# Kernel optimization log

Measured on AMD Instinct MI355X. Metric: run time of the kernel, lower is better.

## Reference

```python
import jax, jax.numpy as jnp
import numpy as np

H, C = 2, 32            # n_heads, hidden_channels (GATv2Conv concat=False -> out dim C)
B, T_PER = 128, 1024    # graphs per batch, tasks per graph
N_TASKS = B * T_PER
N_DATA = 65536
E = 1048576             # edges per relation
N_DEV = 4
TASK_D, DATA_D, DEV_D, EDGE_D = 12, 5, 12, 3


def _leaky(x, s):
    return jnp.where(x >= 0, x, s * x)


def _layernorm(x, g, b):
    m = x.mean(-1, keepdims=True)
    v = x.var(-1, keepdims=True)
    return (x - m) / jnp.sqrt(v + 1e-5) * g + b


def _gatv2(x_src, x_dst, src, dst, Wl, bl, Wr, br, att, Wres, bias, n_dst,
           edge_attr=None, We=None):
    # PyG GATv2Conv: concat=False (mean over heads), residual=True, no self-loops.
    xl = (x_src @ Wl + bl).reshape(-1, H, C)   # [N_src, H, C]
    xr = (x_dst @ Wr + br).reshape(-1, H, C)   # [N_dst, H, C]
    m = xl[src] + xr[dst]                      # [E, H, C]
    if edge_attr is not None:
        m = m + (edge_attr @ We).reshape(-1, H, C)
    e = _leaky(m, 0.2)
    score = jnp.einsum('ehc,hc->eh', e, att)   # [E, H]
    smax = jax.ops.segment_max(score, dst, num_segments=n_dst)
    ex = jnp.exp(score - smax[dst])
    denom = jax.ops.segment_sum(ex, dst, num_segments=n_dst)
    alpha = ex / (denom[dst] + 1e-16)          # segment softmax per destination
    out = jax.ops.segment_sum(alpha[:, :, None] * xl[src], dst, num_segments=n_dst)
    return out.mean(axis=1) + x_dst @ Wres + bias


def setup_inputs() -> dict:
    key = jax.random.key(0)
    ks = iter(jax.random.split(key, 48))
    f = lambda shape: jax.random.normal(next(ks), shape, jnp.float32) * 0.1
    HC = H * C
    inp = {}
    inp['tasks_x'] = jax.random.normal(next(ks), (N_TASKS, TASK_D), jnp.float32)
    inp['data_x'] = jax.random.normal(next(ks), (N_DATA, DATA_D), jnp.float32)
    inp['devices_x'] = jax.random.normal(next(ks), (B * N_DEV, DEV_D), jnp.float32)
    src_dt = jax.random.randint(next(ks), (E,), 0, N_DATA)
    dst_dt = jax.random.randint(next(ks), (E,), 0, N_TASKS)
    inp['edge_index_dt'] = jnp.stack([src_dt, dst_dt])
    inp['edge_attr_dt'] = jax.random.normal(next(ks), (E, EDGE_D), jnp.float32)
    src_tt = jax.random.randint(next(ks), (E,), 0, N_TASKS)
    dst_tt = jax.random.randint(next(ks), (E,), 0, N_TASKS)
    inp['edge_index_tt'] = jnp.stack([src_tt, dst_tt])
    inp['batch'] = jnp.repeat(jnp.arange(B), T_PER)
    inp['ptr'] = jnp.arange(B) * T_PER
    inp['counts'] = jnp.full((B, 1), float(T_PER), jnp.float32)
    # conv1: (data -> tasks), with edge features
    inp['c1_Wl'] = f((DATA_D, HC)); inp['c1_bl'] = jnp.zeros(HC, jnp.float32)
    inp['c1_Wr'] = f((TASK_D, HC)); inp['c1_br'] = jnp.zeros(HC, jnp.float32)
    inp['c1_We'] = f((EDGE_D, HC)); inp['c1_att'] = f((H, C))
    inp['c1_Wres'] = f((TASK_D, C)); inp['c1_bias'] = jnp.zeros(C, jnp.float32)
    # conv2: (tasks -> tasks)
    inp['c2_Wl'] = f((TASK_D, HC)); inp['c2_bl'] = jnp.zeros(HC, jnp.float32)
    inp['c2_Wr'] = f((TASK_D, HC)); inp['c2_br'] = jnp.zeros(HC, jnp.float32)
    inp['c2_att'] = f((H, C))
    inp['c2_Wres'] = f((TASK_D, C)); inp['c2_bias'] = jnp.zeros(C, jnp.float32)
    inp['ln1_g'] = jnp.ones(C, jnp.float32); inp['ln1_b'] = jnp.zeros(C, jnp.float32)
    inp['ln2_g'] = jnp.ones(C, jnp.float32); inp['ln2_b'] = jnp.zeros(C, jnp.float32)
    gat_out = 2 * C + TASK_D                      # 76
    in_head = 2 * gat_out + N_DEV * DEV_D         # 200
    inp['h1_W'] = f((in_head, C)); inp['h1_b'] = jnp.zeros(C, jnp.float32)
    inp['hln_g'] = jnp.ones(C, jnp.float32); inp['hln_b'] = jnp.zeros(C, jnp.float32)
    inp['h2_W'] = f((C, N_DEV - 1)) * 0.01; inp['h2_b'] = jnp.zeros(N_DEV - 1, jnp.float32)
    return inp


def reference(tasks_x, data_x, devices_x, edge_attr_dt, counts,
              c1_Wl, c1_bl, c1_Wr, c1_br, c1_We, c1_att, c1_Wres, c1_bias,
              c2_Wl, c2_bl, c2_Wr, c2_br, c2_att, c2_Wres, c2_bias,
              ln1_g, ln1_b, ln2_g, ln2_b,
              h1_W, h1_b, hln_g, hln_b, h2_W, h2_b,
              edge_index_dt, edge_index_tt, batch, ptr):
    dft = _gatv2(data_x, tasks_x, edge_index_dt[0], edge_index_dt[1],
                 c1_Wl, c1_bl, c1_Wr, c1_br, c1_att, c1_Wres, c1_bias, N_TASKS,
                 edge_attr_dt, c1_We)
    tft = _gatv2(tasks_x, tasks_x, edge_index_tt[0], edge_index_tt[1],
                 c2_Wl, c2_bl, c2_Wr, c2_br, c2_att, c2_Wres, c2_bias, N_TASKS)
    dft = _leaky(_layernorm(dft, ln1_g, ln1_b), 0.01)
    tft = _leaky(_layernorm(tft, ln2_g, ln2_b), 0.01)
    emb = jnp.concatenate([tasks_x, dft, tft], axis=-1)          # [N_TASKS, 76]
    cand = emb[ptr]                                              # candidate per graph
    glob = jax.ops.segment_sum(emb, batch, num_segments=B)       # global_add_pool
    glob = glob / jnp.maximum(counts, 1.0)
    dev = devices_x.reshape(B, N_DEV * DEV_D)
    x = jnp.concatenate([cand, glob, dev], axis=-1)              # [B, 200]
    x = _leaky(_layernorm(x @ h1_W + h1_b, hln_g, hln_b), 0.01)
    return x @ h2_W + h2_b                                       # [B, N_DEV-1]
```

## Files before the change

kernel.cpp:

```cpp
#include <hip/hip_runtime.h>

constexpr int H = 2, C = 32, HC = 64;
constexpr int NB = 128, TPER = 1024;
constexpr int NTASKS = NB * TPER;
constexpr int NDATA = 65536;
constexpr int EE = 1048576;
constexpr int NDEV = 4;
constexpr int TASK_D = 12, DATA_D = 5, DEV_D = 12, EDGE_D = 3;
constexpr int EMB = 2 * C + TASK_D;
constexpr int HEAD_IN = 2 * EMB + NDEV * DEV_D;
constexpr int ND2 = 2 * NTASKS;

constexpr int PSLICES = 256;
constexpr int PSLICE_LEN = 2 * EE / PSLICES;
constexpr int CAP = 32;
constexpr int PACK_BLOCKS = EE / 256;
constexpr int PROJ_BLOCKS = NTASKS / 16;

template <int CTRL>
__device__ __forceinline__ float dpp_addstep(float v) {
    int t = __builtin_amdgcn_update_dpp(0, __float_as_int(v), CTRL, 0xF, 0xF, true);
    return v + __int_as_float(t);
}
__device__ __forceinline__ float sum8(float v) {
    v = dpp_addstep<0xB1>(v);
    v = dpp_addstep<0x4E>(v);
    v = dpp_addstep<0x141>(v);
    return v;
}
__device__ __forceinline__ float sum16(float v) {
    v = sum8(v);
    v = dpp_addstep<0x140>(v);
    return v;
}

__global__ __launch_bounds__(256) void build2_kernel(
        const int* __restrict__ ei_dt,
        const float* __restrict__ data_x, const float* __restrict__ ea,
        float4* __restrict__ epk,
        const float* __restrict__ tx, const float* __restrict__ Wl2,
        const float* __restrict__ bl2, float* __restrict__ xlt2) {
    int b = blockIdx.x;
    if (b < PACK_BLOCKS) {
        int e = b * 256 + threadIdx.x;
        int s = ei_dt[e];
        const float* dp = data_x + (size_t)s * 5;
        float d0 = dp[0], d1 = dp[1], d2 = dp[2], d3 = dp[3], d4 = dp[4];
        float a0 = ea[(size_t)e * 3 + 0];
        float a1 = ea[(size_t)e * 3 + 1];
        float a2 = ea[(size_t)e * 3 + 2];
        epk[(size_t)e * 2 + 0] = make_float4(d0, d1, d2, d3);
        epk[(size_t)e * 2 + 1] = make_float4(d4, a0, a1, a2);
    } else {
        int wave = ((b - PACK_BLOCKS) * 256 + threadIdx.x) >> 6;
        int lane = threadIdx.x & 63;
        float w[12];
#pragma unroll
        for (int k = 0; k < 12; ++k) w[k] = Wl2[k * 64 + lane];
        float bv = bl2[lane];
#pragma unroll
        for (int r = 0; r < 4; ++r) {
            int row = wave * 4 + r;
            const float4* xp = (const float4*)(tx + (size_t)row * 12);
            float4 x0 = xp[0], x1 = xp[1], x2 = xp[2];
            float xf[12] = { x0.x, x0.y, x0.z, x0.w, x1.x, x1.y, x1.z, x1.w,
                             x2.x, x2.y, x2.z, x2.w };
            float a = bv;
#pragma unroll
            for (int k = 0; k < 12; ++k) a = fmaf(xf[k], w[k], a);
            xlt2[(size_t)row * 64 + lane] = a;
        }
    }
}

__global__ __launch_bounds__(256) void scatter_bucket_kernel(
        const int* __restrict__ ei_dt, const int* __restrict__ ei_tt,
        int* __restrict__ cnt, int* __restrict__ bucket) {
    int rr = blockIdx.x & 7;
    int slice = blockIdx.x >> 3;
    int base = slice * PSLICE_LEN;
    bool isc1 = base < EE;
    int dlo = (rr << 14) + (isc1 ? 0 : NTASKS);
    int dhi = dlo + (1 << 14);
    if (isc1) {
        for (int i = threadIdx.x; i < PSLICE_LEN; i += 256) {
            int e = base + i;
            int d = ei_dt[EE + e];
            if (d >= dlo && d < dhi) {
                int pos = atomicAdd(&cnt[d], 1);
                if (pos < CAP) bucket[((size_t)pos << 18) + d] = e;
            }
        }
    } else {
        for (int i = threadIdx.x; i < PSLICE_LEN; i += 256) {
            int ee = base - EE + i;
            int d = NTASKS + ei_tt[EE + ee];
            if (d >= dlo && d < dhi) {
                int pos = atomicAdd(&cnt[d], 1);
                if (pos < CAP) bucket[((size_t)pos << 18) + d] = ei_tt[ee];
            }
        }
    }
}

template <bool HAS_EA>
__global__ __launch_bounds__(256) void gat_gather4_kernel(
        const int* __restrict__ bucket,
        const int* __restrict__ cnt,
        const float4* __restrict__ epk,
        const float* __restrict__ Wl, const float* __restrict__ bl,
        const float* __restrict__ We,
        const float* __restrict__ xlt,
        const float* __restrict__ Wr, const float* __restrict__ br,
        const float* __restrict__ att,
        const float* __restrict__ tx,
        const float* __restrict__ Wres, const float* __restrict__ bias,
        const float* __restrict__ g, const float* __restrict__ bln,
        float* __restrict__ out) {
    int widx = threadIdx.x >> 6;
    int lane = threadIdx.x & 63;
    int grp = lane >> 4;
    int u = lane & 15;
    int rr = blockIdx.x & 7;
    int q = blockIdx.x >> 3;
    int t = (rr << 14) + q * 16 + widx * 4 + grp;

    float4 att4 = ((const float4*)att)[u];
    float4 we0, we1, we2, wl0, wl1, wl2, wl3, wl4, bl4;
    if (HAS_EA) {
        we0 = ((const float4*)We)[u];
        we1 = ((const float4*)(We + 64))[u];
        we2 = ((const float4*)(We + 128))[u];
        wl0 = ((const float4*)(Wl + 0 * 64))[u];
        wl1 = ((const float4*)(Wl + 1 * 64))[u];
        wl2 = ((const float4*)(Wl + 2 * 64))[u];
        wl3 = ((const float4*)(Wl + 3 * 64))[u];
        wl4 = ((const float4*)(Wl + 4 * 64))[u];
        bl4 = ((const float4*)bl)[u];
    }

    const float4* tp = (const float4*)(tx + (size_t)t * 12);
    float4 xr4 = ((const float4*)br)[u];
    {
        float4 t0 = tp[0], t1 = tp[1], t2 = tp[2];
        float tf[12] = { t0.x, t0.y, t0.z, t0.w, t1.x, t1.y, t1.z, t1.w,
                         t2.x, t2.y, t2.z, t2.w };
#pragma unroll
        for (int k = 0; k < 12; ++k) {
            float4 w = ((const float4*)(Wr + k * 64))[u];
            xr4.x = fmaf(tf[k], w.x, xr4.x);
            xr4.y = fmaf(tf[k], w.y, xr4.y);
            xr4.z = fmaf(tf[k], w.z, xr4.z);
            xr4.w = fmaf(tf[k], w.w, xr4.w);
        }
    }

    int len = min(cnt[t], CAP);
    float den = 0.f;
    float4 accv = make_float4(0.f, 0.f, 0.f, 0.f);

    for (int i0 = 0; i0 < len; i0 += 4) {
        int cur[4];
#pragma unroll
        for (int j = 0; j < 4; ++j) {
            int slot = (i0 + j < len) ? (i0 + j) : 0;
            cur[j] = bucket[((size_t)slot << 18) + t];
        }
        float4 gv[4];
        float p[4];
        if (HAS_EA) {
            float4 e0[4], e1[4];
#pragma unroll
            for (int j = 0; j < 4; ++j) {
                e0[j] = epk[(size_t)cur[j] * 2 + 0];
                e1[j] = epk[(size_t)cur[j] * 2 + 1];
            }
#pragma unroll
            for (int j = 0; j < 4; ++j) {
                float4 xl4 = bl4;
                xl4.x = fmaf(e0[j].x, wl0.x, xl4.x); xl4.y = fmaf(e0[j].x, wl0.y, xl4.y);
                xl4.z = fmaf(e0[j].x, wl0.z, xl4.z); xl4.w = fmaf(e0[j].x, wl0.w, xl4.w);
                xl4.x = fmaf(e0[j].y, wl1.x, xl4.x); xl4.y = fmaf(e0[j].y, wl1.y, xl4.y);
                xl4.z = fmaf(e0[j].y, wl1.z, xl4.z); xl4.w = fmaf(e0[j].y, wl1.w, xl4.w);
                xl4.x = fmaf(e0[j].z, wl2.x, xl4.x); xl4.y = fmaf(e0[j].z, wl2.y, xl4.y);
                xl4.z = fmaf(e0[j].z, wl2.z, xl4.z); xl4.w = fmaf(e0[j].z, wl2.w, xl4.w);
                xl4.x = fmaf(e0[j].w, wl3.x, xl4.x); xl4.y = fmaf(e0[j].w, wl3.y, xl4.y);
                xl4.z = fmaf(e0[j].w, wl3.z, xl4.z); xl4.w = fmaf(e0[j].w, wl3.w, xl4.w);
                xl4.x = fmaf(e1[j].x, wl4.x, xl4.x); xl4.y = fmaf(e1[j].x, wl4.y, xl4.y);
                xl4.z = fmaf(e1[j].x, wl4.z, xl4.z); xl4.w = fmaf(e1[j].x, wl4.w, xl4.w);
                gv[j] = xl4;
                float4 m4;
                m4.x = xl4.x + xr4.x; m4.y = xl4.y + xr4.y;
                m4.z = xl4.z + xr4.z; m4.w = xl4.w + xr4.w;
                m4.x = fmaf(e1[j].y, we0.x, fmaf(e1[j].z, we1.x, fmaf(e1[j].w, we2.x, m4.x)));
                m4.y = fmaf(e1[j].y, we0.y, fmaf(e1[j].z, we1.y, fmaf(e1[j].w, we2.y, m4.y)));
                m4.z = fmaf(e1[j].y, we0.z, fmaf(e1[j].z, we1.z, fmaf(e1[j].w, we2.z, m4.z)));
                m4.w = fmaf(e1[j].y, we0.w, fmaf(e1[j].z, we1.w, fmaf(e1[j].w, we2.w, m4.w)));
                float lx = fmaxf(m4.x, 0.f) + 0.2f * fminf(m4.x, 0.f);
                float ly = fmaxf(m4.y, 0.f) + 0.2f * fminf(m4.y, 0.f);
                float lz = fmaxf(m4.z, 0.f) + 0.2f * fminf(m4.z, 0.f);
                float lw = fmaxf(m4.w, 0.f) + 0.2f * fminf(m4.w, 0.f);
                p[j] = fmaf(att4.x, lx, fmaf(att4.y, ly, fmaf(att4.z, lz, att4.w * lw)));
            }
        } else {
#pragma unroll
            for (int j = 0; j < 4; ++j)
                gv[j] = ((const float4*)(xlt + (size_t)cur[j] * 64))[u];
#pragma unroll
            for (int j = 0; j < 4; ++j) {
                float4 m4;
                m4.x = gv[j].x + xr4.x; m4.y = gv[j].y + xr4.y;
                m4.z = gv[j].z + xr4.z; m4.w = gv[j].w + xr4.w;
                float lx = fmaxf(m4.x, 0.f) + 0.2f * fminf(m4.x, 0.f);
                float ly = fmaxf(m4.y, 0.f) + 0.2f * fminf(m4.y, 0.f);
                float lz = fmaxf(m4.z, 0.f) + 0.2f * fminf(m4.z, 0.f);
                float lw = fmaxf(m4.w, 0.f) + 0.2f * fminf(m4.w, 0.f);
                p[j] = fmaf(att4.x, lx, fmaf(att4.y, ly, fmaf(att4.z, lz, att4.w * lw)));
            }
        }
#pragma unroll
        for (int j = 0; j < 4; ++j) p[j] = sum8(p[j]);
#pragma unroll
        for (int j = 0; j < 4; ++j) {
            float ex = __expf(p[j]);
            ex = (i0 + j < len) ? ex : 0.f;
            den += ex;
            accv.x = fmaf(ex, gv[j].x, accv.x);
            accv.y = fmaf(ex, gv[j].y, accv.y);
            accv.z = fmaf(ex, gv[j].z, accv.z);
            accv.w = fmaf(ex, gv[j].w, accv.w);
        }
    }

    float inv = 1.0f / (den + 1e-16f);
    float4 ox = make_float4(accv.x * inv, accv.y * inv, accv.z * inv, accv.w * inv);
    float4 oo;
    oo.x = __shfl_xor(ox.x, 8, 64);
    oo.y = __shfl_xor(ox.y, 8, 64);
    oo.z = __shfl_xor(ox.z, 8, 64);
    oo.w = __shfl_xor(ox.w, 8, 64);
    float4 hm = make_float4(0.5f * (ox.x + oo.x), 0.5f * (ox.y + oo.y),
                            0.5f * (ox.z + oo.z), 0.5f * (ox.w + oo.w));

    float4 r0 = tp[0], r1 = tp[1], r2 = tp[2];
    float tf[12] = { r0.x, r0.y, r0.z, r0.w, r1.x, r1.y, r1.z, r1.w,
                     r2.x, r2.y, r2.z, r2.w };
    int u8 = u & 7;
    float4 bias4 = ((const float4*)bias)[u8];
    float4 v4 = make_float4(hm.x + bias4.x, hm.y + bias4.y,
                            hm.z + bias4.z, hm.w + bias4.w);
#pragma unroll
    for (int k = 0; k < 12; ++k) {
        float4 w = ((const float4*)(Wres + k * 32))[u8];
        v4.x = fmaf(tf[k], w.x, v4.x);
        v4.y = fmaf(tf[k], w.y, v4.y);
        v4.z = fmaf(tf[k], w.z, v4.z);
        v4.w = fmaf(tf[k], w.w, v4.w);
    }
    float loc = v4.x + v4.y + v4.z + v4.w;
    float mean = sum16(loc) * (1.0f / 64.0f);
    float4 dd = make_float4(v4.x - mean, v4.y - mean, v4.z - mean, v4.w - mean);
    float q2l = dd.x * dd.x + dd.y * dd.y + dd.z * dd.z + dd.w * dd.w;
    float var = sum16(q2l) * (1.0f / 64.0f);
    float rs = rsqrtf(var + 1e-5f);
    float4 g4 = ((const float4*)g)[u8];
    float4 b4 = ((const float4*)bln)[u8];
    float4 y;
    y.x = dd.x * rs * g4.x + b4.x;  y.x = (y.x >= 0.f ? y.x : 0.01f * y.x);
    y.y = dd.y * rs * g4.y + b4.y;  y.y = (y.y >= 0.f ? y.y : 0.01f * y.y);
    y.z = dd.z * rs * g4.z + b4.z;  y.z = (y.z >= 0.f ? y.z : 0.01f * y.z);
    y.w = dd.w * rs * g4.w + b4.w;  y.w = (y.w >= 0.f ? y.w : 0.01f * y.w);
    if (u < 8) *((float4*)(out + (size_t)t * 32 + 4 * u8)) = y;
}

__global__ void pool_kernel(const float* __restrict__ tx, const float* __restrict__ dft,
                            const float* __restrict__ tft, float* __restrict__ glob16) {
    int g = blockIdx.x >> 4;
    int ch = blockIdx.x & 15;
    int j = threadIdx.x;
    if (j >= EMB) return;
    int base = g * TPER + ch * 64;
    float s = 0.0f;
    for (int t = 0; t < 64; ++t) {
        int task = base + t;
        float v;
        if (j < 12)      v = tx[(size_t)task * 12 + j];
        else if (j < 44) v = dft[(size_t)task * 32 + (j - 12)];
        else             v = tft[(size_t)task * 32 + (j - 44)];
        s += v;
    }
    glob16[(size_t)blockIdx.x * EMB + j] = s;
}

__global__ void head_kernel(const float* __restrict__ tx, const float* __restrict__ dft,
                            const float* __restrict__ tft, const float* __restrict__ glob16,
                            const float* __restrict__ devx, const float* __restrict__ counts,
                            const int* __restrict__ ptrv,
                            const float* __restrict__ h1_W, const float* __restrict__ h1_b,
                            const float* __restrict__ hln_g, const float* __restrict__ hln_b,
                            const float* __restrict__ h2_W, const float* __restrict__ h2_b,
                            float* __restrict__ out) {
    __shared__ float xs[HEAD_IN];
    __shared__ float ys[32];
    int b = blockIdx.x;
    int l = threadIdx.x;
    int p = ptrv[b];
    float inv = 1.0f / fmaxf(counts[b], 1.0f);
    for (int j = l; j < HEAD_IN; j += 64) {
        float v;
        if (j < 12)       v = tx[(size_t)p * 12 + j];
        else if (j < 44)  v = dft[(size_t)p * 32 + (j - 12)];
        else if (j < 76)  v = tft[(size_t)p * 32 + (j - 44)];
        else if (j < 152) {
            float s = 0.f;
#pragma unroll
            for (int c = 0; c < 16; ++c)
                s += glob16[(size_t)(b * 16 + c) * EMB + (j - 76)];
            v = s * inv;
        }
        else              v = devx[b * (NDEV * DEV_D) + (j - 152)];
        xs[j] = v;
    }
    __syncthreads();
    if (l < 32) {
        float h = h1_b[l];
        for (int k = 0; k < HEAD_IN; ++k)
            h += xs[k] * h1_W[k * 32 + l];
        float s = h;
#pragma unroll
        for (int off = 16; off; off >>= 1) s += __shfl_xor(s, off, 64);
        float mean = s * (1.0f / 32.0f);
        float dd = h - mean;
        float q = dd * dd;
#pragma unroll
        for (int off = 16; off; off >>= 1) q += __shfl_xor(q, off, 64);
        float var = q * (1.0f / 32.0f);
        float y = dd * rsqrtf(var + 1e-5f) * hln_g[l] + hln_b[l];
        ys[l] = (y >= 0.0f ? y : 0.01f * y);
    }
    __syncthreads();
    if (l < NDEV - 1) {
        float o = h2_b[l];
        for (int c = 0; c < 32; ++c)
            o += ys[c] * h2_W[c * 3 + l];
        out[b * (NDEV - 1) + l] = o;
    }
}

extern "C" void kernel_launch(void* const* d_in, const int* in_sizes, int n_in,
                              void* d_out, int out_size, void* d_ws, size_t ws_size,
                              hipStream_t stream) {
    const float* tasks_x   = (const float*)d_in[0];
    const float* data_x    = (const float*)d_in[1];
    const float* devices_x = (const float*)d_in[2];
    const int*   ei_dt     = (const int*)d_in[3];
    const float* ea_dt     = (const float*)d_in[4];
    const int*   ei_tt     = (const int*)d_in[5];
    const int*   ptrv      = (const int*)d_in[7];
    const float* counts    = (const float*)d_in[8];
    const float* c1_Wl   = (const float*)d_in[9];
    const float* c1_bl   = (const float*)d_in[10];
    const float* c1_Wr   = (const float*)d_in[11];
    const float* c1_br   = (const float*)d_in[12];
    const float* c1_We   = (const float*)d_in[13];
    const float* c1_att  = (const float*)d_in[14];
    const float* c1_Wres = (const float*)d_in[15];
    const float* c1_bias = (const float*)d_in[16];
    const float* c2_Wl   = (const float*)d_in[17];
    const float* c2_bl   = (const float*)d_in[18];
    const float* c2_Wr   = (const float*)d_in[19];
    const float* c2_br   = (const float*)d_in[20];
    const float* c2_att  = (const float*)d_in[21];
    const float* c2_Wres = (const float*)d_in[22];
    const float* c2_bias = (const float*)d_in[23];
    const float* ln1_g = (const float*)d_in[24];
    const float* ln1_b = (const float*)d_in[25];
    const float* ln2_g = (const float*)d_in[26];
    const float* ln2_b = (const float*)d_in[27];
    const float* h1_W  = (const float*)d_in[28];
    const float* h1_b  = (const float*)d_in[29];
    const float* hln_g = (const float*)d_in[30];
    const float* hln_b = (const float*)d_in[31];
    const float* h2_W  = (const float*)d_in[32];
    const float* h2_b  = (const float*)d_in[33];
    float* out = (float*)d_out;

    char* ws = (char*)d_ws;
    size_t off = 0;
    auto alloc = [&](size_t bytes) -> void* {
        void* p = (void*)(ws + off);
        off += (bytes + 255) & ~(size_t)255;
        return p;
    };
    int*    cnt     = (int*)alloc((size_t)ND2 * 4);
    int*    bucket  = (int*)alloc((size_t)ND2 * CAP * 4);
    float4* epk     = (float4*)alloc((size_t)EE * 32);
    float*  xlt2    = (float*)alloc((size_t)NTASKS * 64 * 4);
    float*  dft     = (float*)alloc((size_t)NTASKS * 32 * 4);
    float*  tft     = (float*)alloc((size_t)NTASKS * 32 * 4);
    float*  glob16  = (float*)alloc((size_t)NB * 16 * EMB * 4);
    if (off > ws_size) return;

    const int BLK = 256;

    hipMemsetAsync(cnt, 0, (size_t)ND2 * 4, stream);
    scatter_bucket_kernel<<<PSLICES * 8, BLK, 0, stream>>>(ei_dt, ei_tt, cnt, bucket);

    build2_kernel<<<PACK_BLOCKS + PROJ_BLOCKS, BLK, 0, stream>>>(
        ei_dt, data_x, ea_dt, epk, tasks_x, c2_Wl, c2_bl, xlt2);

    gat_gather4_kernel<true><<<NTASKS / 16, BLK, 0, stream>>>(
        bucket, cnt, epk, c1_Wl, c1_bl, c1_We, nullptr,
        c1_Wr, c1_br, c1_att, tasks_x, c1_Wres, c1_bias, ln1_g, ln1_b, dft);

    gat_gather4_kernel<false><<<NTASKS / 16, BLK, 0, stream>>>(
        bucket + NTASKS, cnt + NTASKS, nullptr, nullptr, nullptr, nullptr,
        xlt2, c2_Wr, c2_br, c2_att, tasks_x, c2_Wres, c2_bias, ln2_g, ln2_b, tft);

    pool_kernel<<<NB * 16, 128, 0, stream>>>(tasks_x, dft, tft, glob16);
    head_kernel<<<NB, 64, 0, stream>>>(tasks_x, dft, tft, glob16, devices_x, counts, ptrv,
                                       h1_W, h1_b, hln_g, hln_b, h2_W, h2_b, out);
}
```

Baseline: 284.1 us.

## Replace 8-pass filtered scatter with two-phase binning into destination-range queues

The old scatter had each of 8 block groups scan all edge destinations and keep only those in its 16K-wide destination range, so the edge index was read 8 times. The new code first bins every edge once into 16 global queues keyed by relation and destination range, using a shared-memory histogram and one global atomic per bin per block. A second kernel then drains each queue in chunks and performs the per-destination atomic bucket fill, keeping the atomics localized to a range. This adds an extra kernel and a round trip of int2 queue traffic. The bucket fill order becomes nondeterministic, and entries beyond a queue's fixed capacity are dropped.

```diff
diff --git a/kernel.cpp b/kernel.cpp
--- a/kernel.cpp
+++ b/kernel.cpp
@@ -11,11 +11,14 @@
 constexpr int HEAD_IN = 2 * EMB + NDEV * DEV_D;
 constexpr int ND2 = 2 * NTASKS;
 
-constexpr int PSLICES = 256;
-constexpr int PSLICE_LEN = 2 * EE / PSLICES;
 constexpr int CAP = 32;
 constexpr int PACK_BLOCKS = EE / 256;
 constexpr int PROJ_BLOCKS = NTASKS / 16;
+
+constexpr int EPB = 4096;
+constexpr int BIN_BLOCKS = 2 * EE / EPB;
+constexpr int QSTRIDE = EE / 8 + 8192;
+constexpr int NQB = 32;
 
 template <int CTRL>
 __device__ __forceinline__ float dpp_addstep(float v) {
@@ -73,33 +76,64 @@
     }
 }
 
-__global__ __launch_bounds__(256) void scatter_bucket_kernel(
+__global__ __launch_bounds__(256) void bin_kernel(
         const int* __restrict__ ei_dt, const int* __restrict__ ei_tt,
+        int* __restrict__ qtail, int2* __restrict__ queue) {
+    __shared__ int hist[8], gbase[8], lcur[8];
+    int b = blockIdx.x;
+    int base = b * EPB;
+    bool isc1 = base < EE;
+    const int* dstp = isc1 ? (ei_dt + EE + base) : (ei_tt + EE + (base - EE));
+    if (threadIdx.x < 8) hist[threadIdx.x] = 0;
+    __syncthreads();
+    for (int i = threadIdx.x; i < EPB; i += 256)
+        atomicAdd(&hist[dstp[i] >> 14], 1);
+    __syncthreads();
+    if (threadIdx.x < 8) {
+        int qidx = (isc1 ? 0 : 8) + threadIdx.x;
+        gbase[threadIdx.x] = atomicAdd(&qtail[qidx], hist[threadIdx.x]);
+        lcur[threadIdx.x] = 0;
+    }
+    __syncthreads();
+    if (isc1) {
+        for (int i = threadIdx.x; i < EPB; i += 256) {
+            int d = dstp[i];
+            int rr = d >> 14;
+            int pos = gbase[rr] + atomicAdd(&lcur[rr], 1);
+            if (pos < QSTRIDE)
+                queue[(size_t)rr * QSTRIDE + pos] = make_int2(d, base + i);
+        }
+    } else {
+        for (int i = threadIdx.x; i < EPB; i += 256) {
+            int d = dstp[i];
+            int rr = d >> 14;
+            int pos = gbase[rr] + atomicAdd(&lcur[rr], 1);
+            if (pos < QSTRIDE)
+                queue[(size_t)(8 + rr) * QSTRIDE + pos] =
+                    make_int2(d, ei_tt[base - EE + i]);
+        }
+    }
+}
+
+__global__ __launch_bounds__(256) void scatter_q_kernel(
+        const int* __restrict__ qtail, const int2* __restrict__ queue,
         int* __restrict__ cnt, int* __restrict__ bucket) {
-    int rr = blockIdx.x & 7;
-    int slice = blockIdx.x >> 3;
-    int base = slice * PSLICE_LEN;
-    bool isc1 = base < EE;
-    int dlo = (rr << 14) + (isc1 ? 0 : NTASKS);
-    int dhi = dlo + (1 << 14);
-    if (isc1) {
-        for (int i = threadIdx.x; i < PSLICE_LEN; i += 256) {
-            int e = base + i;
-            int d = ei_dt[EE + e];
-            if (d >= dlo && d < dhi) {
-                int pos = atomicAdd(&cnt[d], 1);
-                if (pos < CAP) bucket[((size_t)pos << 18) + d] = e;
-            }
-        }
-    } else {
-        for (int i = threadIdx.x; i < PSLICE_LEN; i += 256) {
-            int ee = base - EE + i;
-            int d = NTASKS + ei_tt[EE + ee];
-            if (d >= dlo && d < dhi) {
-                int pos = atomicAdd(&cnt[d], 1);
-                if (pos < CAP) bucket[((size_t)pos << 18) + d] = ei_tt[ee];
-            }
-        }
+    int b = blockIdx.x;
+    bool isc1 = b < NQB * 8;
+    int rr = b & 7;
+    int sub = (isc1 ? b : b - NQB * 8) >> 3;
+    int qidx = (isc1 ? 0 : 8) + rr;
+    int qlen = min(qtail[qidx], QSTRIDE);
+    int chunk = (qlen + NQB - 1) / NQB;
+    int lo = sub * chunk;
+    int hi = min(lo + chunk, qlen);
+    const int2* qp = queue + (size_t)qidx * QSTRIDE;
+    int doff = isc1 ? 0 : NTASKS;
+    for (int i = lo + threadIdx.x; i < hi; i += 256) {
+        int2 ent = qp[i];
+        int d = ent.x + doff;
+        int pos = atomicAdd(&cnt[d], 1);
+        if (pos < CAP) bucket[((size_t)pos << 18) + d] = ent.y;
     }
 }
 
@@ -393,7 +427,9 @@
         return p;
     };
     int*    cnt     = (int*)alloc((size_t)ND2 * 4);
+    int*    qtail   = (int*)alloc(16 * 4);
     int*    bucket  = (int*)alloc((size_t)ND2 * CAP * 4);
+    int2*   queue   = (int2*)alloc((size_t)16 * QSTRIDE * 8);
     float4* epk     = (float4*)alloc((size_t)EE * 32);
     float*  xlt2    = (float*)alloc((size_t)NTASKS * 64 * 4);
     float*  dft     = (float*)alloc((size_t)NTASKS * 32 * 4);
@@ -403,8 +439,10 @@
 
     const int BLK = 256;
 
-    hipMemsetAsync(cnt, 0, (size_t)ND2 * 4, stream);
-    scatter_bucket_kernel<<<PSLICES * 8, BLK, 0, stream>>>(ei_dt, ei_tt, cnt, bucket);
+    hipMemsetAsync(cnt, 0, (size_t)ND2 * 4 + 256, stream);
+    bin_kernel<<<BIN_BLOCKS, BLK, 0, stream>>>(ei_dt, ei_tt, qtail, queue);
+
+    scatter_q_kernel<<<NQB * 8 * 2, BLK, 0, stream>>>(qtail, queue, cnt, bucket);
 
     build2_kernel<<<PACK_BLOCKS + PROJ_BLOCKS, BLK, 0, stream>>>(
         ei_dt, data_x, ea_dt, epk, tasks_x, c2_Wl, c2_bl, xlt2);
```

Result: slower. 341.5 us (+20.2%).
